# Kernel tuning notes

Hardware: AMD Instinct MI355X
Metric: run time of the kernel (lower is better)

## Reference

```python
import jax, jax.numpy as jnp
import numpy as np

B, S, D, H, HD = 2, 2048, 2048, 16, 128  # batch, seq, embed, heads, head_dim


def setup_inputs() -> dict:
    key = jax.random.key(0)
    k0, k1, k2 = jax.random.split(key, 3)
    hidden_states = jax.random.normal(k0, (B, S, D), dtype=jnp.float32)
    # fused QKV projection: [D, H*HD + 2*HD] (multi-query: single shared K and V head)
    W_attn = jax.random.normal(k1, (D, H * HD + 2 * HD), dtype=jnp.float32) * 0.02
    b_attn = jnp.zeros((H * HD + 2 * HD,), dtype=jnp.float32)
    W_proj = jax.random.normal(k2, (D, D), dtype=jnp.float32) * 0.02
    b_proj = jnp.zeros((D,), dtype=jnp.float32)
    # causal mask, broadcastable to (B, Q, H, K); True = attend
    attention_mask = jnp.tril(jnp.ones((S, S), dtype=bool))[None, :, None, :]
    return {
        "hidden_states": hidden_states,
        "W_attn": W_attn,
        "b_attn": b_attn,
        "W_proj": W_proj,
        "b_proj": b_proj,
        "attention_mask": attention_mask,
    }


def reference(hidden_states, W_attn, b_attn, W_proj, b_proj, attention_mask):
    # fused QKV, then split into Q (H heads) and shared K/V (multi-query)
    qkv = hidden_states @ W_attn + b_attn          # (B, S, H*HD + 2*HD)
    q = qkv[..., : H * HD].reshape(B, S, H, HD)    # (B, Q, H, hd)
    key_t = qkv[..., H * HD : H * HD + HD]         # (B, K, hd) shared K head
    value = qkv[..., H * HD + HD :]                # (B, K, hd) shared V head

    # dtype == softmax_dtype (fp32) -> upcast=False, unscale=1
    scale_factor = 1.0 / (HD ** 0.5)               # scale_attn_weights
    attn_weights = jnp.einsum("bqhd,bkd->bqhk", q, key_t) * scale_factor
    mask_value = jnp.finfo(jnp.float32).min
    attn_weights = jnp.where(attention_mask, attn_weights, mask_value)
    attn_weights = jax.nn.softmax(attn_weights, axis=-1)

    attn_output = jnp.einsum("bqhk,bkd->bqhd", attn_weights, value)
    attn_output = attn_output.reshape(B, S, H * HD)
    return attn_output @ W_proj + b_proj           # (B, S, D)
```

## Files before the change

kernel.cpp:

```cpp
#include <hip/hip_runtime.h>
#include <math.h>

constexpr int cB  = 2;
constexpr int cS  = 2048;
constexpr int cD  = 2048;
constexpr int cH  = 16;
constexpr int cHD = 128;
constexpr int cNQKV = cH * cHD + 2 * cHD;

typedef __attribute__((ext_vector_type(8))) short bf16x8;
typedef __attribute__((ext_vector_type(4))) float f32x4;
typedef __attribute__((ext_vector_type(16))) float f32x16;

__device__ __forceinline__ short f2bf(float f) {
    union { float f; unsigned u; } v; v.f = f;
    unsigned r = (v.u + 0x7FFFu + ((v.u >> 16) & 1u)) >> 16;
    return (short)r;
}

__device__ __forceinline__ unsigned pk_bf16(float lo, float hi_) {
    return (unsigned)(unsigned short)f2bf(lo)
         | ((unsigned)(unsigned short)f2bf(hi_) << 16);
}

typedef __attribute__((address_space(3))) void lds_t;
typedef const __attribute__((address_space(1))) void gbl_t;
__device__ __forceinline__ void gld16(const void* g, void* l) {
    __builtin_amdgcn_global_load_lds((gbl_t*)g, (lds_t*)l, 16, 0, 0);
}

__global__ __launch_bounds__(256) void conv_bf16(
    const float* __restrict__ src, short* __restrict__ dst)
{
    size_t i = ((size_t)blockIdx.x * 256 + threadIdx.x) * 8;
    float4 a = *(const float4*)(src + i);
    float4 b = *(const float4*)(src + i + 4);
    bf16x8 o;
    o[0] = f2bf(a.x); o[1] = f2bf(a.y); o[2] = f2bf(a.z); o[3] = f2bf(a.w);
    o[4] = f2bf(b.x); o[5] = f2bf(b.y); o[6] = f2bf(b.z); o[7] = f2bf(b.w);
    *(bf16x8*)(dst + i) = o;
}

__global__ __launch_bounds__(256) void transpose_bf16(
    const float* __restrict__ src, short* __restrict__ dst, int K, int N)
{
    __shared__ short t[32][33];
    const int n0 = blockIdx.x * 32, k0 = blockIdx.y * 32;
    const int x = threadIdx.x & 31, y = threadIdx.x >> 5;
#pragma unroll
    for (int i = 0; i < 4; ++i)
        t[y + 8 * i][x] = f2bf(src[(size_t)(k0 + y + 8 * i) * N + n0 + x]);
    __syncthreads();
#pragma unroll
    for (int i = 0; i < 4; ++i)
        dst[(size_t)(n0 + y + 8 * i) * K + k0 + x] = t[x][y + 8 * i];
}

template<bool BF16_OUT>
__global__ __launch_bounds__(256) void gemm_mfma(
    const short* __restrict__ A, const short* __restrict__ Bt,
    const float* __restrict__ bias, void* __restrict__ Cout,
    int M, int N, int K, float qscale, int qcols)
{
    __shared__ short As[128 * 32];
    __shared__ short Bs[128 * 32];

    const int tid = threadIdx.x;
    const int lane = tid & 63, n16 = lane & 15, quad = lane >> 4;
    const int wave = tid >> 6, wm = wave >> 1, wn = wave & 1;
    const int m0 = blockIdx.y * 128, n0 = blockIdx.x * 128;

    f32x4 acc[4][4];
#pragma unroll
    for (int i = 0; i < 4; ++i)
#pragma unroll
        for (int j = 0; j < 4; ++j) acc[i][j] = 0.0f;

    const int s0 = tid, s1 = tid + 256;
    const short* Ag0 = A  + (size_t)(m0 + (s0 >> 2)) * K + (s0 & 3) * 8;
    const short* Ag1 = A  + (size_t)(m0 + (s1 >> 2)) * K + (s1 & 3) * 8;
    const short* Bg0 = Bt + (size_t)(n0 + (s0 >> 2)) * K + (s0 & 3) * 8;
    const short* Bg1 = Bt + (size_t)(n0 + (s1 >> 2)) * K + (s1 & 3) * 8;

    for (int k0 = 0; k0 < K; k0 += 32) {
        gld16(Ag0 + k0, &As[s0 * 8]);
        gld16(Ag1 + k0, &As[s1 * 8]);
        gld16(Bg0 + k0, &Bs[s0 * 8]);
        gld16(Bg1 + k0, &Bs[s1 * 8]);
        __syncthreads();
        bf16x8 af[4], bfr[4];
#pragma unroll
        for (int mt = 0; mt < 4; ++mt)
            af[mt] = *(const bf16x8*)&As[(wm * 64 + mt * 16 + n16) * 32 + quad * 8];
#pragma unroll
        for (int nt = 0; nt < 4; ++nt)
            bfr[nt] = *(const bf16x8*)&Bs[(wn * 64 + nt * 16 + n16) * 32 + quad * 8];
#pragma unroll
        for (int mt = 0; mt < 4; ++mt)
#pragma unroll
            for (int nt = 0; nt < 4; ++nt)
                acc[mt][nt] = __builtin_amdgcn_mfma_f32_16x16x32_bf16(
                    af[mt], bfr[nt], acc[mt][nt], 0, 0, 0);
        __syncthreads();
    }

#pragma unroll
    for (int nt = 0; nt < 4; ++nt) {
        const int col = n0 + wn * 64 + nt * 16 + n16;
        const float bv = bias[col];
        const float sc = (col < qcols) ? qscale : 1.0f;
#pragma unroll
        for (int mt = 0; mt < 4; ++mt)
#pragma unroll
            for (int r = 0; r < 4; ++r) {
                const int row = m0 + wm * 64 + mt * 16 + quad * 4 + r;
                const float v = (acc[mt][nt][r] + bv) * sc;
                if (BF16_OUT) ((short*)Cout)[(size_t)row * N + col] = f2bf(v);
                else          ((float*)Cout)[(size_t)row * N + col] = v;
            }
    }
}

__global__ __launch_bounds__(256) void prep_v(
    const short* __restrict__ qkvb, short* __restrict__ Vt)
{
    const int b  = blockIdx.y;
    const int k0 = blockIdx.x * 64;
    const int t  = threadIdx.x;
#pragma unroll
    for (int i = 0; i < 32; ++i) {
        int idx = i * 256 + t;
        int hd = idx >> 6, key = idx & 63;
        Vt[((size_t)b * cHD + hd) * cS + k0 + key] =
            qkvb[((size_t)(b * cS + k0 + key)) * cNQKV + cH * cHD + cHD + hd];
    }
}

__global__ __launch_bounds__(128) void attn_mfma(
    const short* __restrict__ qkvb, const short* __restrict__ Vt,
    short* __restrict__ out)
{
    const int tid  = threadIdx.x;
    const int wave = tid >> 6;
    const int lane = tid & 63;
    const int q32  = lane & 31;
    const int hi   = lane >> 5;
    const int h  = blockIdx.y;
    const int b  = blockIdx.z;

    __shared__ __align__(16) short Ks[2][64 * 128];
    __shared__ __align__(16) short Vs[2][128 * 64];
    __shared__ __align__(16) float Linv[2][32];

    const short* kglob = qkvb + (size_t)b * cS * cNQKV + cH * cHD;
    const short* vbase = Vt + (size_t)b * cHD * cS;

    const int kl = lane >> 4;
    const int kx = (lane & 15) * 16;
    const int vdl = lane >> 3;
    const int vx  = (lane & 7) * 16;

    int cur = 0;

    auto stage = [&](int buf, int k0) {
#pragma unroll
        for (int j = 0; j < 8; ++j) {
            const int keyt = (wave * 8 + j) * 4 + kl;
            const int srcb = kx ^ ((keyt & 15) << 4);
            gld16((const char*)(kglob + (size_t)(k0 + keyt) * cNQKV) + srcb,
                  &Ks[buf][(wave * 8 + j) * 512]);
        }
#pragma unroll
        for (int j = 0; j < 8; ++j) {
            const int d = (wave * 8 + j) * 8 + vdl;
            const int srcb = vx ^ ((d & 7) << 4);
            gld16((const char*)(vbase + (size_t)d * cS + k0) + srcb,
                  &Vs[buf][(wave * 8 + j) * 512]);
        }
    };

#pragma unroll 1
    for (int seg = 0; seg < 2; ++seg) {
        const int qt = seg ? (int)blockIdx.x : 31 - (int)blockIdx.x;
        const int qb = qt * 64;
        const int qg = qb + wave * 32 + q32;
        const int nkt = qt + 1;

        bf16x8 qf[8];
        {
            const short* qbase = qkvb + ((size_t)(b * cS) + qg) * cNQKV
                               + h * cHD + hi * 8;
#pragma unroll
            for (int dblk = 0; dblk < 8; ++dblk)
                qf[dblk] = *(const bf16x8*)(qbase + dblk * 16);
        }

        f32x16 oc[4];
#pragma unroll
        for (int i = 0; i < 4; ++i) oc[i] = 0.0f;
        float lp = 0.0f;

        __syncthreads();
        stage(cur, 0);

#pragma unroll 1
        for (int kt = 0; kt < nkt; ++kt) {
            const int k0 = kt * 64;
            __syncthreads();
            if (kt + 1 < nkt) stage(cur ^ 1, k0 + 64);

            f32x16 sc[2];
            sc[0] = 0.0f; sc[1] = 0.0f;
            __builtin_amdgcn_s_setprio(1);
#pragma unroll
            for (int kt2 = 0; kt2 < 2; ++kt2) {
                const int key = kt2 * 32 + q32;
                const char* krow = (const char*)&Ks[cur][key * 128];
                const int swz = (key & 15) << 4;
#pragma unroll
                for (int dblk = 0; dblk < 8; ++dblk) {
                    bf16x8 kf = *(const bf16x8*)(krow + ((dblk * 32 + hi * 16) ^ swz));
                    sc[kt2] = __builtin_amdgcn_mfma_f32_32x32x16_bf16(
                        kf, qf[dblk], sc[kt2], 0, 0, 0);
                }
            }
            __builtin_amdgcn_s_setprio(0);

            const bool diag = (kt == nkt - 1);
            float e[2][16];
#pragma unroll
            for (int kt2 = 0; kt2 < 2; ++kt2)
#pragma unroll
                for (int r = 0; r < 16; ++r) {
                    float s = sc[kt2][r];
                    if (diag) {
                        int kgl = k0 + kt2 * 32 + (r & 3) + 8 * (r >> 2) + 4 * hi;
                        if (kgl > qg) s = -1e30f;
                    }
                    float p = __expf(s);
                    lp += p;
                    e[kt2][r] = p;
                }

            bf16x8 pa[4];
#pragma unroll
            for (int kblk = 0; kblk < 4; ++kblk) {
                const int kt2 = kblk >> 1;
                const int rb  = 8 * (kblk & 1);
                unsigned wA0 = pk_bf16(e[kt2][rb + 0], e[kt2][rb + 1]);
                unsigned wA1 = pk_bf16(e[kt2][rb + 2], e[kt2][rb + 3]);
                unsigned wB0 = pk_bf16(e[kt2][rb + 4], e[kt2][rb + 5]);
                unsigned wB1 = pk_bf16(e[kt2][rb + 6], e[kt2][rb + 7]);
                unsigned keep0 = hi ? wB0 : wA0, keep1 = hi ? wB1 : wA1;
                unsigned send0 = hi ? wA0 : wB0, send1 = hi ? wA1 : wB1;
                unsigned recv0 = (unsigned)__shfl_xor((int)send0, 32);
                unsigned recv1 = (unsigned)__shfl_xor((int)send1, 32);
                union { unsigned u[4]; bf16x8 v; } uu;
                uu.u[0] = hi ? recv0 : keep0;
                uu.u[1] = hi ? recv1 : keep1;
                uu.u[2] = hi ? keep0 : recv0;
                uu.u[3] = hi ? keep1 : recv1;
                pa[kblk] = uu.v;
            }

            __builtin_amdgcn_s_setprio(1);
#pragma unroll
            for (int kblk = 0; kblk < 4; ++kblk)
#pragma unroll
                for (int dtile = 0; dtile < 4; ++dtile) {
                    const int d = dtile * 32 + q32;
                    const char* vrow = (const char*)&Vs[cur][d * 64];
                    bf16x8 vf = *(const bf16x8*)(vrow + ((kblk * 32 + hi * 16) ^ ((d & 7) << 4)));
                    oc[dtile] = __builtin_amdgcn_mfma_f32_32x32x16_bf16(
                        pa[kblk], vf, oc[dtile], 0, 0, 0);
                }
            __builtin_amdgcn_s_setprio(0);

            cur ^= 1;
        }

        lp += __shfl_xor(lp, 32);
        if (hi == 0) Linv[wave][q32] = 1.0f / lp;
        __syncthreads();
        f32x4 invv[4];
#pragma unroll
        for (int g = 0; g < 4; ++g)
            invv[g] = *(const f32x4*)&Linv[wave][g * 8 + hi * 4];

        short* obase = out + ((size_t)(b * cS) + qb + wave * 32) * cD + h * cHD;
#pragma unroll
        for (int dtile = 0; dtile < 4; ++dtile)
#pragma unroll
            for (int r = 0; r < 16; ++r) {
                const int q = (r & 3) + 8 * (r >> 2) + 4 * hi;
                obase[(size_t)q * cD + dtile * 32 + q32] =
                    f2bf(oc[dtile][r] * invv[r >> 2][r & 3]);
            }
    }
}

extern "C" void kernel_launch(void* const* d_in, const int* in_sizes, int n_in,
                              void* d_out, int out_size, void* d_ws, size_t ws_size,
                              hipStream_t stream)
{
    const float* hidden = (const float*)d_in[0];
    const float* W_attn = (const float*)d_in[1];
    const float* b_attn = (const float*)d_in[2];
    const float* W_proj = (const float*)d_in[3];
    const float* b_proj = (const float*)d_in[4];
    float* out = (float*)d_out;

    const int M = cB * cS;
    short* qkvb = (short*)d_ws;
    short* Ah   = qkvb + (size_t)M * cNQKV;
    short* Wb   = Ah   + (size_t)M * cD;
    short* Wpb  = Wb   + (size_t)cNQKV * cD;
    short* Vt   = Wpb  + (size_t)cD * cD;
    short* attno = Ah;

    const float scale = 0.088388347648318447f;

    conv_bf16<<<(size_t)M * cD / 2048, 256, 0, stream>>>(hidden, Ah);
    transpose_bf16<<<dim3(cNQKV / 32, cD / 32), 256, 0, stream>>>(W_attn, Wb, cD, cNQKV);
    transpose_bf16<<<dim3(cD / 32, cD / 32), 256, 0, stream>>>(W_proj, Wpb, cD, cD);

    gemm_mfma<true><<<dim3(cNQKV / 128, M / 128), 256, 0, stream>>>(
        Ah, Wb, b_attn, qkvb, M, cNQKV, cD, scale, cH * cHD);

    prep_v<<<dim3(cS / 64, cB), 256, 0, stream>>>(qkvb, Vt);

    attn_mfma<<<dim3(16, cH, cB), 128, 0, stream>>>(qkvb, Vt, attno);

    gemm_mfma<false><<<dim3(cD / 128, M / 128), 256, 0, stream>>>(
        attno, Wpb, b_proj, out, M, cD, cD, 1.0f, 0);
}
```

Measured before the change: 346.9 us.

## Split attention key tile across four waves and reduce partial outputs in LDS

The attention block grows from two waves to four. Each pair of waves now covers one 32-query half and one 32-key half of each 64-key tile, so per-wave MFMA work per tile is halved and more waves are available to hide latency. At the end, partial O accumulators and row sums from the second key half are written to LDS, reusing the K/V buffers, and added in by the first half before normalization. This costs extra syncthreads and an LDS reduction pass per segment, and the 256-thread launch bound with two blocks per CU may constrain registers.

```diff
diff --git a/kernel.cpp b/kernel.cpp
--- a/kernel.cpp
+++ b/kernel.cpp
@@ -136,7 +136,7 @@
     }
 }
 
-__global__ __launch_bounds__(128) void attn_mfma(
+__global__ __launch_bounds__(256, 2) void attn_mfma(
     const short* __restrict__ qkvb, const short* __restrict__ Vt,
     short* __restrict__ out)
 {
@@ -145,12 +145,16 @@
     const int lane = tid & 63;
     const int q32  = lane & 31;
     const int hi   = lane >> 5;
+    const int qhalf = wave & 1;
+    const int khalf = wave >> 1;
     const int h  = blockIdx.y;
     const int b  = blockIdx.z;
 
     __shared__ __align__(16) short Ks[2][64 * 128];
     __shared__ __align__(16) short Vs[2][128 * 64];
     __shared__ __align__(16) float Linv[2][32];
+    float* Obuf = (float*)Ks;
+    float* Lbuf = (float*)Vs;
 
     const short* kglob = qkvb + (size_t)b * cS * cNQKV + cH * cHD;
     const short* vbase = Vt + (size_t)b * cHD * cS;
@@ -164,18 +168,20 @@
 
     auto stage = [&](int buf, int k0) {
 #pragma unroll
-        for (int j = 0; j < 8; ++j) {
-            const int keyt = (wave * 8 + j) * 4 + kl;
+        for (int j = 0; j < 4; ++j) {
+            const int i = wave * 4 + j;
+            const int keyt = i * 4 + kl;
             const int srcb = kx ^ ((keyt & 15) << 4);
             gld16((const char*)(kglob + (size_t)(k0 + keyt) * cNQKV) + srcb,
-                  &Ks[buf][(wave * 8 + j) * 512]);
-        }
-#pragma unroll
-        for (int j = 0; j < 8; ++j) {
-            const int d = (wave * 8 + j) * 8 + vdl;
+                  &Ks[buf][i * 512]);
+        }
+#pragma unroll
+        for (int j = 0; j < 4; ++j) {
+            const int i = wave * 4 + j;
+            const int d = i * 8 + vdl;
             const int srcb = vx ^ ((d & 7) << 4);
             gld16((const char*)(vbase + (size_t)d * cS + k0) + srcb,
-                  &Vs[buf][(wave * 8 + j) * 512]);
+                  &Vs[buf][i * 512]);
         }
     };
 
@@ -183,7 +189,7 @@
     for (int seg = 0; seg < 2; ++seg) {
         const int qt = seg ? (int)blockIdx.x : 31 - (int)blockIdx.x;
         const int qb = qt * 64;
-        const int qg = qb + wave * 32 + q32;
+        const int qg = qb + qhalf * 32 + q32;
         const int nkt = qt + 1;
 
         bf16x8 qf[8];
@@ -209,48 +215,43 @@
             __syncthreads();
             if (kt + 1 < nkt) stage(cur ^ 1, k0 + 64);
 
-            f32x16 sc[2];
-            sc[0] = 0.0f; sc[1] = 0.0f;
-            __builtin_amdgcn_s_setprio(1);
-#pragma unroll
-            for (int kt2 = 0; kt2 < 2; ++kt2) {
-                const int key = kt2 * 32 + q32;
+            f32x16 sc = 0.0f;
+            {
+                const int key = khalf * 32 + q32;
                 const char* krow = (const char*)&Ks[cur][key * 128];
                 const int swz = (key & 15) << 4;
+                __builtin_amdgcn_s_setprio(1);
 #pragma unroll
                 for (int dblk = 0; dblk < 8; ++dblk) {
                     bf16x8 kf = *(const bf16x8*)(krow + ((dblk * 32 + hi * 16) ^ swz));
-                    sc[kt2] = __builtin_amdgcn_mfma_f32_32x32x16_bf16(
-                        kf, qf[dblk], sc[kt2], 0, 0, 0);
-                }
+                    sc = __builtin_amdgcn_mfma_f32_32x32x16_bf16(
+                        kf, qf[dblk], sc, 0, 0, 0);
+                }
+                __builtin_amdgcn_s_setprio(0);
             }
-            __builtin_amdgcn_s_setprio(0);
 
             const bool diag = (kt == nkt - 1);
-            float e[2][16];
-#pragma unroll
-            for (int kt2 = 0; kt2 < 2; ++kt2)
-#pragma unroll
-                for (int r = 0; r < 16; ++r) {
-                    float s = sc[kt2][r];
-                    if (diag) {
-                        int kgl = k0 + kt2 * 32 + (r & 3) + 8 * (r >> 2) + 4 * hi;
-                        if (kgl > qg) s = -1e30f;
-                    }
-                    float p = __expf(s);
-                    lp += p;
-                    e[kt2][r] = p;
-                }
-
-            bf16x8 pa[4];
-#pragma unroll
-            for (int kblk = 0; kblk < 4; ++kblk) {
-                const int kt2 = kblk >> 1;
-                const int rb  = 8 * (kblk & 1);
-                unsigned wA0 = pk_bf16(e[kt2][rb + 0], e[kt2][rb + 1]);
-                unsigned wA1 = pk_bf16(e[kt2][rb + 2], e[kt2][rb + 3]);
-                unsigned wB0 = pk_bf16(e[kt2][rb + 4], e[kt2][rb + 5]);
-                unsigned wB1 = pk_bf16(e[kt2][rb + 6], e[kt2][rb + 7]);
+            float e[16];
+#pragma unroll
+            for (int r = 0; r < 16; ++r) {
+                float s = sc[r];
+                if (diag) {
+                    int kgl = k0 + khalf * 32 + (r & 3) + 8 * (r >> 2) + 4 * hi;
+                    if (kgl > qg) s = -1e30f;
+                }
+                float p = __expf(s);
+                lp += p;
+                e[r] = p;
+            }
+
+            bf16x8 pa[2];
+#pragma unroll
+            for (int kblk = 0; kblk < 2; ++kblk) {
+                const int rb = 8 * kblk;
+                unsigned wA0 = pk_bf16(e[rb + 0], e[rb + 1]);
+                unsigned wA1 = pk_bf16(e[rb + 2], e[rb + 3]);
+                unsigned wB0 = pk_bf16(e[rb + 4], e[rb + 5]);
+                unsigned wB1 = pk_bf16(e[rb + 6], e[rb + 7]);
                 unsigned keep0 = hi ? wB0 : wA0, keep1 = hi ? wB1 : wA1;
                 unsigned send0 = hi ? wA0 : wB0, send1 = hi ? wA1 : wB1;
                 unsigned recv0 = (unsigned)__shfl_xor((int)send0, 32);
@@ -265,12 +266,13 @@
 
             __builtin_amdgcn_s_setprio(1);
 #pragma unroll
-            for (int kblk = 0; kblk < 4; ++kblk)
+            for (int kblk = 0; kblk < 2; ++kblk)
 #pragma unroll
                 for (int dtile = 0; dtile < 4; ++dtile) {
                     const int d = dtile * 32 + q32;
                     const char* vrow = (const char*)&Vs[cur][d * 64];
-                    bf16x8 vf = *(const bf16x8*)(vrow + ((kblk * 32 + hi * 16) ^ ((d & 7) << 4)));
+                    bf16x8 vf = *(const bf16x8*)(vrow +
+                        ((khalf * 64 + kblk * 32 + hi * 16) ^ ((d & 7) << 4)));
                     oc[dtile] = __builtin_amdgcn_mfma_f32_32x32x16_bf16(
                         pa[kblk], vf, oc[dtile], 0, 0, 0);
                 }
@@ -280,22 +282,47 @@
         }
 
         lp += __shfl_xor(lp, 32);
-        if (hi == 0) Linv[wave][q32] = 1.0f / lp;
-        __syncthreads();
-        f32x4 invv[4];
-#pragma unroll
-        for (int g = 0; g < 4; ++g)
-            invv[g] = *(const f32x4*)&Linv[wave][g * 8 + hi * 4];
-
-        short* obase = out + ((size_t)(b * cS) + qb + wave * 32) * cD + h * cHD;
-#pragma unroll
-        for (int dtile = 0; dtile < 4; ++dtile)
-#pragma unroll
-            for (int r = 0; r < 16; ++r) {
-                const int q = (r & 3) + 8 * (r >> 2) + 4 * hi;
-                obase[(size_t)q * cD + dtile * 32 + q32] =
-                    f2bf(oc[dtile][r] * invv[r >> 2][r & 3]);
-            }
+        __syncthreads();
+        if (khalf == 1) {
+            float* ob = Obuf + qhalf * 32 * 128;
+#pragma unroll
+            for (int dtile = 0; dtile < 4; ++dtile)
+#pragma unroll
+                for (int r = 0; r < 16; ++r) {
+                    const int q = (r & 3) + 8 * (r >> 2) + 4 * hi;
+                    ob[q * 128 + dtile * 32 + q32] = oc[dtile][r];
+                }
+            if (hi == 0) Lbuf[qhalf * 32 + q32] = lp;
+        }
+        __syncthreads();
+        if (khalf == 0) {
+            float* ob = Obuf + qhalf * 32 * 128;
+#pragma unroll
+            for (int dtile = 0; dtile < 4; ++dtile)
+#pragma unroll
+                for (int r = 0; r < 16; ++r) {
+                    const int q = (r & 3) + 8 * (r >> 2) + 4 * hi;
+                    oc[dtile][r] += ob[q * 128 + dtile * 32 + q32];
+                }
+            lp += Lbuf[qhalf * 32 + q32];
+            if (hi == 0) Linv[qhalf][q32] = 1.0f / lp;
+        }
+        __syncthreads();
+        if (khalf == 0) {
+            f32x4 invv[4];
+#pragma unroll
+            for (int g = 0; g < 4; ++g)
+                invv[g] = *(const f32x4*)&Linv[qhalf][g * 8 + hi * 4];
+            short* obase = out + ((size_t)(b * cS) + qb + qhalf * 32) * cD + h * cHD;
+#pragma unroll
+            for (int dtile = 0; dtile < 4; ++dtile)
+#pragma unroll
+                for (int r = 0; r < 16; ++r) {
+                    const int q = (r & 3) + 8 * (r >> 2) + 4 * hi;
+                    obase[(size_t)q * cD + dtile * 32 + q32] =
+                        f2bf(oc[dtile][r] * invv[r >> 2][r & 3]);
+                }
+        }
     }
 }
 
@@ -329,7 +356,7 @@
 
     prep_v<<<dim3(cS / 64, cB), 256, 0, stream>>>(qkvb, Vt);
 
-    attn_mfma<<<dim3(16, cH, cB), 128, 0, stream>>>(qkvb, Vt, attno);
+    attn_mfma<<<dim3(16, cH, cB), 256, 0, stream>>>(qkvb, Vt, attno);
 
     gemm_mfma<false><<<dim3(cD / 128, M / 128), 256, 0, stream>>>(
         attno, Wpb, b_proj, out, M, cD, cD, 1.0f, 0);
```

Result: faster. 336.5 us (-3.0%).
